# Optimization experiments

Hardware: AMD Instinct MI355X
Metric: run time of the kernel (lower is better)

## Reference

```python
import jax, jax.numpy as jnp
import numpy as np

B, S, D, H = 8, 1024, 1024, 16
DK = D // H


def setup_inputs() -> dict:
    key = jax.random.key(0)
    ks = jax.random.split(key, 12)
    sc = 1.0 / np.sqrt(D)
    return {
        "query": jax.random.normal(ks[0], (B, S, D), jnp.float32),
        "key": jax.random.normal(ks[1], (B, S, D), jnp.float32),
        "value": jax.random.normal(ks[2], (B, S, D), jnp.float32),
        "Wq": jax.random.normal(ks[3], (D, D), jnp.float32) * sc,
        "bq": jnp.zeros((D,), jnp.float32),
        "Wk": jax.random.normal(ks[4], (D, D), jnp.float32) * sc,
        "bk": jnp.zeros((D,), jnp.float32),
        "Wv": jax.random.normal(ks[5], (D, D), jnp.float32) * sc,
        "bv": jnp.zeros((D,), jnp.float32),
        "Wa": jax.random.normal(ks[6], (D, D), jnp.float32) * sc,
        "ba": jnp.zeros((D,), jnp.float32),
        "qvec": jax.random.normal(ks[7], (D,), jnp.float32),
    }


def reference(query, key, value, Wq, bq, Wk, bk, Wv, bv, Wa, ba, qvec):
    # project and split heads: [B,S,D] -> [B,H,S,DK]
    def split(x, W, b):
        y = x @ W.T + b
        return y.reshape(B, S, H, DK).transpose(0, 2, 1, 3)

    q = split(query, Wq, bq)
    k = split(key, Wk, bk)
    v = split(value, Wv, bv)

    scores = jnp.einsum('bhqd,bhkd->bhqk', q, k) / jnp.sqrt(jnp.float32(DK))
    p = jax.nn.softmax(scores, axis=-1)          # dropout p=0 -> identity
    x = jnp.einsum('bhqk,bhkd->bhqd', p, v)
    x = x.transpose(0, 2, 1, 3).reshape(B, S, D)  # [B,S,D]

    # attention2 pooling head
    a = jnp.tanh(x @ Wa.T + ba) @ qvec           # [B,S]
    alpha = jax.nn.softmax(a, axis=-1)
    return jnp.einsum('bs,bsd->bd', alpha, x)    # [B,D]
```

## Files before the change

### kernel.cpp

```cpp
#include <hip/hip_runtime.h>

typedef __bf16 bf16;
typedef __attribute__((ext_vector_type(8))) __bf16 bf16x8;
typedef __attribute__((ext_vector_type(4))) __bf16 bf16x4;
typedef __attribute__((ext_vector_type(4))) float f32x4;

#define GLDS16(g, l) __builtin_amdgcn_global_load_lds( \
    (const __attribute__((address_space(1))) void*)(g), \
    (__attribute__((address_space(3))) void*)(l), 16, 0, 0)

#define MFMA16(a, b, c) __builtin_amdgcn_mfma_f32_16x16x32_bf16(a, b, c, 0, 0, 0)

#define TR16(dst, addr, off) \
  asm volatile("ds_read_b64_tr_b16 %0, %1 offset:" #off : "=v"(dst) : "v"(addr))

struct CvtAll { const float* in[7]; bf16* out[7]; };

__global__ __launch_bounds__(256) void f2b_all(CvtAll a) {
  const int i = blockIdx.x * 256 + threadIdx.x;
  const float* in;
  bf16* out;
  int off;
  if (blockIdx.y < 3) {
    in = a.in[blockIdx.y];
    out = a.out[blockIdx.y];
    off = i;
  } else {
    if (i >= 524288) return;
    const int widx = 3 + (i >> 17);
    in = a.in[widx];
    out = a.out[widx];
    off = i & 131071;
  }
  const f32x4* p = (const f32x4*)in + (size_t)off * 2;
  f32x4 x = p[0], y = p[1];
  bf16x8 o;
  o[0] = (bf16)x[0]; o[1] = (bf16)x[1]; o[2] = (bf16)x[2]; o[3] = (bf16)x[3];
  o[4] = (bf16)y[0]; o[5] = (bf16)y[1]; o[6] = (bf16)y[2]; o[7] = (bf16)y[3];
  ((bf16x8*)out)[off] = o;
}

template <int EPI>
__device__ __forceinline__ void gemm_body8(
    const bf16* __restrict__ A, const bf16* __restrict__ Bw,
    const float* __restrict__ bias, const float* __restrict__ qv,
    bf16* __restrict__ C, float* __restrict__ part,
    const int row0, const int col0, const int N, const int K) {
  __shared__ __attribute__((aligned(16))) bf16 L[2][4][8192];
  const int tid = threadIdx.x;
  const int wid = tid >> 6, lane = tid & 63;
  const int g = lane >> 4, lc = lane & 15;
  const int wr = wid >> 2, wc = wid & 3;

  const bf16* gA = A + (size_t)(row0 + (tid & 255)) * K + (tid >> 8) * 8;
  const bf16* gB = Bw + (size_t)(col0 + (tid & 255)) * K + (tid >> 8) * 8;
  const int d0 = (tid - lane) * 8;

#define STG_A(T, kh) do { \
    const bf16* gp_ = gA + (T) * 64 + (kh) * 32; \
    bf16* lp_ = &L[(T) & 1][(kh)][d0]; \
    GLDS16(gp_, lp_); GLDS16(gp_ + 16, lp_ + 4096); } while (0)
#define STG_B(T, kh) do { \
    const bf16* gp_ = gB + (T) * 64 + (kh) * 32; \
    bf16* lp_ = &L[(T) & 1][2 + (kh)][d0]; \
    GLDS16(gp_, lp_); GLDS16(gp_ + 16, lp_ + 4096); } while (0)
#define RD_A(c, kh) do { \
    _Pragma("unroll") for (int m_ = 0; m_ < 8; ++m_) \
      af[m_] = *(const bf16x8*)&L[c][kh][(g * 256 + wr * 128 + m_ * 16 + lc) * 8]; \
  } while (0)
#define RD_B(c, kh, nh) do { \
    bf[0] = *(const bf16x8*)&L[c][2 + (kh)][(g * 256 + wc * 64 + (nh) * 32 + lc) * 8]; \
    bf[1] = *(const bf16x8*)&L[c][2 + (kh)][(g * 256 + wc * 64 + (nh) * 32 + 16 + lc) * 8]; \
  } while (0)
#define BARS \
    __builtin_amdgcn_s_barrier(); \
    asm volatile("s_waitcnt lgkmcnt(0)" ::: "memory"); \
    __builtin_amdgcn_sched_barrier(0);
#define MM(nh) do { \
    __builtin_amdgcn_s_setprio(1); \
    _Pragma("unroll") for (int m_ = 0; m_ < 8; ++m_) { \
      acc[m_][(nh) * 2 + 0] = MFMA16(af[m_], bf[0], acc[m_][(nh) * 2 + 0]); \
      acc[m_][(nh) * 2 + 1] = MFMA16(af[m_], bf[1], acc[m_][(nh) * 2 + 1]); \
    } \
    __builtin_amdgcn_s_setprio(0); } while (0)
#define ENDP do { \
    __builtin_amdgcn_s_barrier(); \
    asm volatile("" ::: "memory"); \
    __builtin_amdgcn_sched_barrier(0); } while (0)

  const f32x4 z4 = {0.f, 0.f, 0.f, 0.f};
  f32x4 acc[8][4];
#pragma unroll
  for (int m = 0; m < 8; ++m)
#pragma unroll
    for (int n = 0; n < 4; ++n) acc[m][n] = z4;

  bf16x8 af[8], bf[2];
  const int NT = K >> 6;
  const int NI = NT >> 1;

  STG_A(0, 0); STG_B(0, 0); STG_A(0, 1); STG_B(0, 1);
  STG_A(1, 0); STG_B(1, 0); STG_A(1, 1);
  asm volatile("s_waitcnt vmcnt(6)" ::: "memory");
  ENDP;

  for (int i = 0; i < NI; ++i) {
    const int t1 = 2 * i + 1, t2 = 2 * i + 2, t3 = 2 * i + 3;
    const bool p2 = t2 < NT, p3 = t3 < NT;
    RD_A(0, 0); RD_B(0, 0, 0);
    STG_B(t1, 1);
    BARS; MM(0); ENDP;
    RD_B(0, 0, 1);
    if (p2) STG_A(t2, 0);
    BARS; MM(1); ENDP;
    RD_A(0, 1); RD_B(0, 1, 0);
    if (p2) STG_B(t2, 0);
    BARS; MM(0); ENDP;
    RD_B(0, 1, 1);
    if (p2) STG_A(t2, 1);
    BARS; MM(1);
    if (p2) { asm volatile("s_waitcnt vmcnt(6)" ::: "memory"); }
    else    { asm volatile("s_waitcnt vmcnt(0)" ::: "memory"); }
    ENDP;
    RD_A(1, 0); RD_B(1, 0, 0);
    if (p2) STG_B(t2, 1);
    BARS; MM(0); ENDP;
    RD_B(1, 0, 1);
    if (p3) STG_A(t3, 0);
    BARS; MM(1); ENDP;
    RD_A(1, 1); RD_B(1, 1, 0);
    if (p3) STG_B(t3, 0);
    BARS; MM(0); ENDP;
    RD_B(1, 1, 1);
    if (p3) STG_A(t3, 1);
    BARS; MM(1);
    asm volatile("s_waitcnt vmcnt(6)" ::: "memory");
    ENDP;
  }

#undef STG_A
#undef STG_B
#undef RD_A
#undef RD_B
#undef BARS
#undef MM
#undef ENDP

  if constexpr (EPI == 0) {
#pragma unroll
    for (int n = 0; n < 4; ++n) {
      const int col = col0 + wc * 64 + n * 16 + lc;
      const float bb = bias[col];
#pragma unroll
      for (int m = 0; m < 8; ++m)
#pragma unroll
        for (int r = 0; r < 4; ++r) {
          const int row = row0 + wr * 128 + m * 16 + g * 4 + r;
          C[(size_t)row * N + col] = (bf16)(acc[m][n][r] + bb);
        }
    }
  } else {
    float ps[8][4];
#pragma unroll
    for (int m = 0; m < 8; ++m)
#pragma unroll
      for (int r = 0; r < 4; ++r) ps[m][r] = 0.f;
#pragma unroll
    for (int n = 0; n < 4; ++n) {
      const int col = col0 + wc * 64 + n * 16 + lc;
      const float bb = bias[col];
      const float qq = qv[col];
#pragma unroll
      for (int m = 0; m < 8; ++m)
#pragma unroll
        for (int r = 0; r < 4; ++r)
          ps[m][r] += tanhf(acc[m][n][r] + bb) * qq;
    }
    float* pdst = part + (size_t)((col0 >> 8) * 4 + wc) * 8192;
#pragma unroll
    for (int m = 0; m < 8; ++m)
#pragma unroll
      for (int r = 0; r < 4; ++r) {
        float v = ps[m][r];
        v += __shfl_xor(v, 1); v += __shfl_xor(v, 2);
        v += __shfl_xor(v, 4); v += __shfl_xor(v, 8);
        if (lc == 0) {
          const int row = row0 + wr * 128 + m * 16 + g * 4 + r;
          pdst[row] = v;
        }
      }
  }
}

__device__ __forceinline__ void swz128(int phys, int& row0, int& col0) {
  const int lg = (phys & 7) * 16 + (phys >> 3);
  row0 = (lg >> 2) * 256;
  col0 = (lg & 3) * 256;
}

struct GemmSet { const bf16* A; const bf16* Bw; const float* bias; bf16* C; };
struct Gemm3Args { GemmSet s[3]; };

__global__ __launch_bounds__(512, 2) void gemm3_kernel(Gemm3Args a) {
  const GemmSet s = a.s[blockIdx.y];
  int row0, col0;
  swz128(blockIdx.x, row0, col0);
  gemm_body8<0>(s.A, s.Bw, s.bias, nullptr, s.C, nullptr, row0, col0, 1024, 1024);
}

__global__ __launch_bounds__(512, 2) void gemm_a_kernel(
    const bf16* __restrict__ A, const bf16* __restrict__ Bw,
    const float* __restrict__ bias, const float* __restrict__ qv,
    float* __restrict__ part) {
  int row0, col0;
  swz128(blockIdx.x, row0, col0);
  gemm_body8<1>(A, Bw, bias, qv, nullptr, part, row0, col0, 1024, 1024);
}

__global__ __launch_bounds__(256) void attn_kernel(
    const bf16* __restrict__ qp, const bf16* __restrict__ kp,
    const bf16* __restrict__ vp, bf16* __restrict__ xb, float* __restrict__ xf) {
  constexpr int S = 1024, D = 1024;
  __shared__ __attribute__((aligned(16))) bf16 Ks[8192];
  __shared__ __attribute__((aligned(16))) bf16 Vs[8192];
  __shared__ __attribute__((aligned(16))) bf16 Ps[4096];
  const int tid = threadIdx.x, wid = tid >> 6, lane = tid & 63;
  const int g = lane >> 4, lc = lane & 15;
  const int b = blockIdx.x >> 4, h = blockIdx.x & 15;
  const int q0 = blockIdx.y * 64;
  const size_t base = (size_t)b * S * D + (size_t)h * 64;

  bf16x8 qf[2];
  {
    const bf16* qrow = qp + base + (size_t)(q0 + wid * 16 + lc) * D;
    qf[0] = *(const bf16x8*)(qrow + g * 8);
    qf[1] = *(const bf16x8*)(qrow + 32 + g * 8);
#pragma unroll
    for (int j = 0; j < 8; ++j) {
      qf[0][j] = (bf16)((float)qf[0][j] * 0.125f);
      qf[1][j] = (bf16)((float)qf[1][j] * 0.125f);
    }
  }
  float m_s = -1e30f, l_s = 0.f;
  const f32x4 z4 = {0.f, 0.f, 0.f, 0.f};
  f32x4 ax[4];
#pragma unroll
  for (int m = 0; m < 4; ++m) ax[m] = z4;

  const int c0 = tid, c1 = tid + 256;
  const bf16* gK0 = kp + base + (size_t)(c0 & 63) * D + (c0 >> 6) * 8;
  const bf16* gK1 = kp + base + (size_t)(c1 & 63) * D + (c1 >> 6) * 8;
  bf16* lK0 = Ks + (size_t)(c0 - lane) * 8;
  bf16* lK1 = Ks + (size_t)(c1 - lane) * 8;
  const bf16* gV0 = vp + base + (size_t)((c0 >> 5) * 4 + ((c0 >> 1) & 3)) * D +
                    ((c0 >> 3) & 3) * 16 + (c0 & 1) * 8;
  const bf16* gV1 = vp + base + (size_t)((c1 >> 5) * 4 + ((c1 >> 1) & 3)) * D +
                    ((c1 >> 3) & 3) * 16 + (c1 & 1) * 8;
  bf16* lV0 = Vs + (size_t)(c0 - lane) * 8;
  bf16* lV1 = Vs + (size_t)(c1 - lane) * 8;

  bf16* pw = Ps + wid * 1024;
  const int pswz_a = lc & 3, pswz_b = (lc >> 2) & 3;
  const unsigned vaddr0 =
      (unsigned)(uintptr_t)(const __attribute__((address_space(3))) bf16*)(Vs + 512 * g + 4 * lc);

  GLDS16(gK0, lK0);
  GLDS16(gK1, lK1);
  GLDS16(gV0, lV0);
  GLDS16(gV1, lV1);

  for (int t = 0; t < 16; ++t) {
    __syncthreads();
    const int cur = t & 1;
    if (t < 15) {
      const size_t off = (size_t)(t + 1) * 64 * D;
      const int nb = cur ^ 1;
      GLDS16(gK0 + off, lK0 + nb * 4096);
      GLDS16(gK1 + off, lK1 + nb * 4096);
      GLDS16(gV0 + off, lV0 + nb * 4096);
      GLDS16(gV1 + off, lV1 + nb * 4096);
    }
    const bf16* Kb = Ks + cur * 4096;
    const unsigned va = vaddr0 + cur * 8192u;

    f32x4 sc[4];
    __builtin_amdgcn_s_setprio(1);
#pragma unroll
    for (int m = 0; m < 4; ++m) {
      f32x4 z = z4;
      bf16x8 kf0 = *(const bf16x8*)(Kb + (size_t)g * 512 + (m * 16 + lc) * 8);
      bf16x8 kf1 = *(const bf16x8*)(Kb + (size_t)(4 + g) * 512 + (m * 16 + lc) * 8);
      z = MFMA16(kf0, qf[0], z);
      z = MFMA16(kf1, qf[1], z);
      sc[m] = z;
    }
    __builtin_amdgcn_s_setprio(0);

    float mx = -1e30f;
#pragma unroll
    for (int m = 0; m < 4; ++m)
      mx = fmaxf(mx, fmaxf(fmaxf(sc[m][0], sc[m][1]), fmaxf(sc[m][2], sc[m][3])));
    mx = fmaxf(mx, __shfl_xor(mx, 16));
    mx = fmaxf(mx, __shfl_xor(mx, 32));
    if (!__all(mx - m_s <= 8.f)) {
      const float mn = fmaxf(m_s, mx);
      const float cr = __expf(m_s - mn);
      l_s *= cr;
#pragma unroll
      for (int m = 0; m < 4; ++m) ax[m] *= cr;
      m_s = mn;
    }
    float sm = 0.f;
#pragma unroll
    for (int m = 0; m < 4; ++m)
#pragma unroll
      for (int r = 0; r < 4; ++r) {
        float p = __expf(sc[m][r] - m_s);
        sc[m][r] = p;
        sm += p;
      }
    sm += __shfl_xor(sm, 16);
    sm += __shfl_xor(sm, 32);
    l_s += sm;

#pragma unroll
    for (int m = 0; m < 4; ++m) {
      bf16x4 pk;
      pk[0] = (bf16)sc[m][0]; pk[1] = (bf16)sc[m][1];
      pk[2] = (bf16)sc[m][2]; pk[3] = (bf16)sc[m][3];
      *(bf16x4*)(pw + lc * 64 + 16 * (m ^ pswz_a) + 4 * (g ^ pswz_b)) = pk;
    }

    bf16x4 pr[2][2];
#pragma unroll
    for (int kk = 0; kk < 2; ++kk)
#pragma unroll
      for (int jh = 0; jh < 2; ++jh) {
        const int msrc = 2 * kk + (g >> 1);
        const int gsrc = (2 * g + jh) & 3;
        pr[kk][jh] = *(const bf16x4*)(pw + lc * 64 + 16 * (msrc ^ pswz_a) + 4 * (gsrc ^ pswz_b));
      }
    bf16x8 pf0 = __builtin_shufflevector(pr[0][0], pr[0][1], 0, 1, 2, 3, 4, 5, 6, 7);
    bf16x8 pf1 = __builtin_shufflevector(pr[1][0], pr[1][1], 0, 1, 2, 3, 4, 5, 6, 7);

    bf16x4 vt[4][2][2];
    TR16(vt[0][0][0], va, 0);    TR16(vt[1][0][0], va, 128);
    TR16(vt[2][0][0], va, 256);  TR16(vt[3][0][0], va, 384);
    TR16(vt[0][0][1], va, 512);  TR16(vt[1][0][1], va, 640);
    TR16(vt[2][0][1], va, 768);  TR16(vt[3][0][1], va, 896);
    TR16(vt[0][1][0], va, 4096); TR16(vt[1][1][0], va, 4224);
    TR16(vt[2][1][0], va, 4352); TR16(vt[3][1][0], va, 4480);
    TR16(vt[0][1][1], va, 4608); TR16(vt[1][1][1], va, 4736);
    TR16(vt[2][1][1], va, 4864); TR16(vt[3][1][1], va, 4992);
    asm volatile("s_waitcnt lgkmcnt(0)" ::: "memory");
    __builtin_amdgcn_sched_barrier(0);

    __builtin_amdgcn_s_setprio(1);
#pragma unroll
    for (int md = 0; md < 4; ++md) {
      bf16x8 a0 = __builtin_shufflevector(vt[md][0][0], vt[md][0][1], 0, 1, 2, 3, 4, 5, 6, 7);
      bf16x8 a1 = __builtin_shufflevector(vt[md][1][0], vt[md][1][1], 0, 1, 2, 3, 4, 5, 6, 7);
      ax[md] = MFMA16(a0, pf0, ax[md]);
      ax[md] = MFMA16(a1, pf1, ax[md]);
    }
    __builtin_amdgcn_s_setprio(0);
  }

  const float inv = 1.0f / l_s;
  const int qrow = q0 + wid * 16 + lc;
  float* xfr = xf + base + (size_t)qrow * D;
  bf16* xbr = xb + base + (size_t)qrow * D;
#pragma unroll
  for (int m = 0; m < 4; ++m) {
    f32x4 vv = ax[m] * inv;
    *(f32x4*)(xfr + 16 * m + 4 * g) = vv;
    bf16x4 bb;
    bb[0] = (bf16)vv[0]; bb[1] = (bf16)vv[1];
    bb[2] = (bf16)vv[2]; bb[3] = (bf16)vv[3];
    *(bf16x4*)(xbr + 16 * m + 4 * g) = bb;
  }
}

__global__ __launch_bounds__(256) void alphapool_kernel(
    const float* __restrict__ part, const float* __restrict__ xf,
    float* __restrict__ out) {
  __shared__ float alpha[1024];
  __shared__ float red[8];
  const int b = blockIdx.x, t = threadIdx.x;

  f32x4 a4 = {0.f, 0.f, 0.f, 0.f};
#pragma unroll
  for (int p = 0; p < 16; ++p) {
    const float* pp = part + (size_t)p * 8192 + b * 1024 + t * 4;
    a4[0] += pp[0]; a4[1] += pp[1]; a4[2] += pp[2]; a4[3] += pp[3];
  }
  float m = fmaxf(fmaxf(a4[0], a4[1]), fmaxf(a4[2], a4[3]));
#pragma unroll
  for (int o = 1; o < 64; o <<= 1) m = fmaxf(m, __shfl_xor(m, o));
  if ((t & 63) == 0) red[t >> 6] = m;
  __syncthreads();
  m = fmaxf(fmaxf(red[0], red[1]), fmaxf(red[2], red[3]));
  f32x4 e;
  float s = 0.f;
#pragma unroll
  for (int j = 0; j < 4; ++j) { e[j] = __expf(a4[j] - m); s += e[j]; }
#pragma unroll
  for (int o = 1; o < 64; o <<= 1) s += __shfl_xor(s, o);
  if ((t & 63) == 0) red[4 + (t >> 6)] = s;
  __syncthreads();
  const float inv = 1.0f / (red[4] + red[5] + red[6] + red[7]);
  *(f32x4*)(alpha + t * 4) = e * inv;
  __syncthreads();

  f32x4 acc0 = {0.f, 0.f, 0.f, 0.f}, acc1 = {0.f, 0.f, 0.f, 0.f};
  const float* xrow = xf + (size_t)b * 1024 * 1024 + t * 4;
  for (int s2 = 0; s2 < 1024; s2 += 2) {
    acc0 += alpha[s2] * *(const f32x4*)(xrow + (size_t)s2 * 1024);
    acc1 += alpha[s2 + 1] * *(const f32x4*)(xrow + (size_t)(s2 + 1) * 1024);
  }
  *(f32x4*)(out + b * 1024 + t * 4) = acc0 + acc1;
}

extern "C" void kernel_launch(void* const* d_in, const int* in_sizes, int n_in,
                              void* d_out, int out_size, void* d_ws, size_t ws_size,
                              hipStream_t stream) {
  const float* Q   = (const float*)d_in[0];
  const float* K   = (const float*)d_in[1];
  const float* V   = (const float*)d_in[2];
  const float* Wq  = (const float*)d_in[3];
  const float* bq  = (const float*)d_in[4];
  const float* Wk  = (const float*)d_in[5];
  const float* bk  = (const float*)d_in[6];
  const float* Wv  = (const float*)d_in[7];
  const float* bv  = (const float*)d_in[8];
  const float* Wa  = (const float*)d_in[9];
  const float* ba  = (const float*)d_in[10];
  const float* qvec = (const float*)d_in[11];
  float* out = (float*)d_out;
  char* ws = (char*)d_ws;
  const size_t MB = 1ull << 20;

  bf16* Wqb = (bf16*)(ws + 0 * MB);
  bf16* Wkb = (bf16*)(ws + 2 * MB);
  bf16* Wvb = (bf16*)(ws + 4 * MB);
  bf16* Wab = (bf16*)(ws + 6 * MB);
  bf16* qb  = (bf16*)(ws + 8 * MB);
  bf16* kb  = (bf16*)(ws + 24 * MB);
  bf16* vb  = (bf16*)(ws + 40 * MB);
  bf16* qp  = (bf16*)(ws + 56 * MB);
  bf16* kp  = (bf16*)(ws + 72 * MB);
  bf16* vp  = (bf16*)(ws + 88 * MB);
  float* part = (float*)(ws + 104 * MB);
  bf16* xb  = qb;
  float* xf = (float*)(ws + 24 * MB);

  CvtAll cv = {{Q, K, V, Wq, Wk, Wv, Wa}, {qb, kb, vb, Wqb, Wkb, Wvb, Wab}};
  f2b_all<<<dim3(4096, 4), 256, 0, stream>>>(cv);

  Gemm3Args g3 = {{{qb, Wqb, bq, qp}, {kb, Wkb, bk, kp}, {vb, Wvb, bv, vp}}};
  gemm3_kernel<<<dim3(128, 3), 512, 0, stream>>>(g3);

  attn_kernel<<<dim3(128, 16), 256, 0, stream>>>(qp, kp, vp, xb, xf);

  gemm_a_kernel<<<128, 512, 0, stream>>>(xb, Wab, ba, qvec, part);

  alphapool_kernel<<<8, 256, 0, stream>>>(part, xf, out);
}
```

Baseline: 296.8 us.

## Split alpha-pooling into softmax kernel and parallel atomic pooling over sequence chunks

Moves the softmax over the pooling logits into its own kernel that writes alpha to workspace. The weighted sum over the sequence is spread across 128 blocks (16 sequence chunks per batch) and combined with float atomicAdd into a zeroed output. This targets the old 8-block reduction, which read 32 MB of fp32 activations using very few CUs. The cost is an extra memset and launch, and atomic accumulation whose summation order is nondeterministic.

```diff
diff --git a/kernel.cpp b/kernel.cpp
--- a/kernel.cpp
+++ b/kernel.cpp
@@ -381,13 +381,10 @@
   }
 }
 
-__global__ __launch_bounds__(256) void alphapool_kernel(
-    const float* __restrict__ part, const float* __restrict__ xf,
-    float* __restrict__ out) {
-  __shared__ float alpha[1024];
+__global__ __launch_bounds__(256) void softmax_part(const float* __restrict__ part,
+                                                    float* __restrict__ alpha) {
   __shared__ float red[8];
   const int b = blockIdx.x, t = threadIdx.x;
-
   f32x4 a4 = {0.f, 0.f, 0.f, 0.f};
 #pragma unroll
   for (int p = 0; p < 16; ++p) {
@@ -409,16 +406,24 @@
   if ((t & 63) == 0) red[4 + (t >> 6)] = s;
   __syncthreads();
   const float inv = 1.0f / (red[4] + red[5] + red[6] + red[7]);
-  *(f32x4*)(alpha + t * 4) = e * inv;
-  __syncthreads();
-
-  f32x4 acc0 = {0.f, 0.f, 0.f, 0.f}, acc1 = {0.f, 0.f, 0.f, 0.f};
-  const float* xrow = xf + (size_t)b * 1024 * 1024 + t * 4;
-  for (int s2 = 0; s2 < 1024; s2 += 2) {
-    acc0 += alpha[s2] * *(const f32x4*)(xrow + (size_t)s2 * 1024);
-    acc1 += alpha[s2 + 1] * *(const f32x4*)(xrow + (size_t)(s2 + 1) * 1024);
-  }
-  *(f32x4*)(out + b * 1024 + t * 4) = acc0 + acc1;
+  *(f32x4*)(alpha + b * 1024 + t * 4) = e * inv;
+}
+
+__global__ __launch_bounds__(256) void pool_kernel(const float* __restrict__ xf,
+                                                   const float* __restrict__ alpha,
+                                                   float* __restrict__ out) {
+  const int b = blockIdx.y, sc = blockIdx.x, t = threadIdx.x;
+  f32x4 acc = {0.f, 0.f, 0.f, 0.f};
+  const float* xrow = xf + (size_t)b * 1024 * 1024;
+  for (int s = sc * 64; s < sc * 64 + 64; ++s) {
+    const float al = alpha[b * 1024 + s];
+    f32x4 xv = *(const f32x4*)(xrow + (size_t)s * 1024 + t * 4);
+    acc += xv * al;
+  }
+  atomicAdd(&out[b * 1024 + t * 4 + 0], acc[0]);
+  atomicAdd(&out[b * 1024 + t * 4 + 1], acc[1]);
+  atomicAdd(&out[b * 1024 + t * 4 + 2], acc[2]);
+  atomicAdd(&out[b * 1024 + t * 4 + 3], acc[3]);
 }
 
 extern "C" void kernel_launch(void* const* d_in, const int* in_sizes, int n_in,
@@ -450,10 +455,13 @@
   bf16* qp  = (bf16*)(ws + 56 * MB);
   bf16* kp  = (bf16*)(ws + 72 * MB);
   bf16* vp  = (bf16*)(ws + 88 * MB);
-  float* part = (float*)(ws + 104 * MB);
+  float* part  = (float*)(ws + 104 * MB);
+  float* alpha = (float*)(ws + 104 * MB + 524288);
   bf16* xb  = qb;
   float* xf = (float*)(ws + 24 * MB);
 
+  hipMemsetAsync(out, 0, 8192 * sizeof(float), stream);
+
   CvtAll cv = {{Q, K, V, Wq, Wk, Wv, Wa}, {qb, kb, vb, Wqb, Wkb, Wvb, Wab}};
   f2b_all<<<dim3(4096, 4), 256, 0, stream>>>(cv);
 
@@ -464,5 +472,6 @@
 
   gemm_a_kernel<<<128, 512, 0, stream>>>(xb, Wab, ba, qvec, part);
 
-  alphapool_kernel<<<8, 256, 0, stream>>>(part, xf, out);
-}
+  softmax_part<<<8, 256, 0, stream>>>(part, alpha);
+  pool_kernel<<<dim3(16, 8), 256, 0, stream>>>(xf, alpha, out);
+}
```

After: 263.2 us. 1.13x faster.
